# Kernel optimization log

Measured on AMD Instinct MI355X. Metric: run time of the kernel, lower is better.

Reference implementation:

```python
import jax, jax.numpy as jnp
import numpy as np

B, T, D, E, H, K = 4, 4096, 1024, 8, 512, 2  # batch, seq, n_embed, num_experts, bottleneck, top_k


def setup_inputs() -> dict:
    key = jax.random.key(0)
    ks = jax.random.split(key, 8)
    s = 0.02  # param scale (original zero-inits adapters; random used for a meaningful baseline)
    return {
        "x": jax.random.normal(ks[0], (B, T, D), jnp.float32),
        "Wr": (jax.random.normal(ks[1], (D, E), jnp.float32) * s),
        "br": jnp.zeros((E,), jnp.float32),
        "Wn": (jax.random.normal(ks[2], (D, E), jnp.float32) * s),
        "bn": jnp.zeros((E,), jnp.float32),
        "Wd": (jax.random.normal(ks[3], (E, D, H), jnp.float32) * s),
        "bd": jnp.zeros((E, H), jnp.float32),
        "Wu": (jax.random.normal(ks[4], (E, H, D), jnp.float32) * s),
        "bu": jnp.zeros((E, D), jnp.float32),
        "noise": jax.random.normal(ks[5], (B, T, E), jnp.float32),
        "top_k": K,
    }


def reference(x, Wr, br, Wn, bn, Wd, bd, Wu, bu, noise, top_k):
    # --- NoisyTopkRouter ---
    logits = x @ Wr + br                                   # [B,T,E]
    noise_logits = x @ Wn + bn                             # [B,T,E]
    noisy = logits + noise * jax.nn.softplus(noise_logits)  # randn * softplus(noise_logits)
    _, idx = jax.lax.top_k(noisy, top_k)                   # [B,T,K]
    # mask of selected experts; where(mask, noisy, -inf) == scatter(top_k_logits into -inf)
    mask = jax.nn.one_hot(idx, noisy.shape[-1], dtype=jnp.bool_).any(axis=-2)  # [B,T,E]
    sparse = jnp.where(mask, noisy, -jnp.inf)
    gates = jax.nn.softmax(sparse, axis=-1)                # zeros for unselected experts

    # --- Experts (dense grouped form; gate==0 exactly kills unselected experts incl. biases) ---
    down = jnp.einsum('btd,edh->bteh', x, Wd) + bd         # [B,T,E,H]
    hidden = jax.nn.gelu(down, approximate=False)          # torch GELU is exact (erf)
    up = jnp.einsum('bteh,ehd->bted', hidden, Wu) + bu     # [B,T,E,D]
    return jnp.einsum('bted,bte->btd', up, gates)          # gate-weighted combine
```

## Files before the change

### kernel.cpp

```cpp
#include <hip/hip_runtime.h>
#include <hip/hip_bf16.h>
#include <hip/hip_fp16.h>
#include <math.h>

#define DD   1024
#define EE   8
#define HH   512
#define NTOK 16384
#define MAXMT 40
#define NSL_D 4
#define NSL_U 8
#define NWD  (EE * MAXMT * NSL_D)
#define NWU  (EE * MAXMT * NSL_U)

typedef __attribute__((ext_vector_type(8))) short short8;
typedef __attribute__((ext_vector_type(4))) float floatx4;

__device__ __forceinline__ ushort f2bfu(float f) {
    __hip_bfloat16 h = __float2bfloat16(f);
    return *reinterpret_cast<ushort*>(&h);
}
__device__ __forceinline__ float bfu2f(ushort u) {
    union { unsigned u; float f; } cv; cv.u = ((unsigned)u) << 16; return cv.f;
}

__device__ __forceinline__ void glds16(const void* g, void* l) {
    __builtin_amdgcn_global_load_lds(
        (const __attribute__((address_space(1))) unsigned int*)g,
        (__attribute__((address_space(3))) unsigned int*)l, 16, 0, 0);
}

__global__ __launch_bounds__(256) void trans_k(const float* __restrict__ src, ushort* __restrict__ dst,
                                               const int R, const int C, int* __restrict__ cnt) {
    if (cnt && blockIdx.x == 0 && blockIdx.y == 0 && blockIdx.z == 0 && threadIdx.x < 256)
        cnt[threadIdx.x] = 0;
    const int e = blockIdx.z, r0 = blockIdx.y * 64, c0 = blockIdx.x * 64;
    __shared__ float t[64][65];
    const int tid = threadIdx.x;
    const int cseg = (tid & 15) * 4, rr = tid >> 4;
#pragma unroll
    for (int j = 0; j < 4; ++j) {
        const int r = rr + j * 16;
        const float4 v = *(const float4*)(src + ((size_t)e * R + r0 + r) * C + c0 + cseg);
        t[r][cseg] = v.x; t[r][cseg+1] = v.y; t[r][cseg+2] = v.z; t[r][cseg+3] = v.w;
    }
    __syncthreads();
    const int rseg = (tid & 15) * 4;
#pragma unroll
    for (int j = 0; j < 4; ++j) {
        const int crow = (tid >> 4) + j * 16;
        ushort o[4];
#pragma unroll
        for (int q = 0; q < 4; ++q) o[q] = f2bfu(t[rseg + q][crow]);
        *(uint2*)(dst + ((size_t)e * C + c0 + crow) * R + r0 + rseg) = *(uint2*)o;
    }
}

__device__ __forceinline__ void route_token(
    const float* ar, const float* an, int t,
    const float* __restrict__ br, const float* __restrict__ bn,
    const float* __restrict__ noise,
    unsigned& e0, unsigned& p0, unsigned& e1, unsigned& p1)
{
    float noisy[EE];
#pragma unroll
    for (int e = 0; e < EE; ++e) {
        const float lg = ar[e] + br[e];
        const float nl = an[e] + bn[e];
        const float sp = fmaxf(nl, 0.f) + log1pf(expf(-fabsf(nl)));
        noisy[e] = lg + noise[(size_t)t * EE + e] * sp;
    }
    int i0 = 0;
#pragma unroll
    for (int e = 1; e < EE; ++e) if (noisy[e] > noisy[i0]) i0 = e;
    int i1 = (i0 == 0) ? 1 : 0;
#pragma unroll
    for (int e = 0; e < EE; ++e) if (e != i0 && noisy[e] > noisy[i1]) i1 = e;
    const float ex = expf(noisy[i1] - noisy[i0]);
    const float g0 = 1.f / (1.f + ex);
    const float g1 = ex / (1.f + ex);
    __half h0 = __float2half_rn(g0), h1 = __float2half_rn(g1);
    e0 = (unsigned)i0;
    e1 = (unsigned)i1;
    p0 = (unsigned)t | ((unsigned)*reinterpret_cast<ushort*>(&h0) << 16);
    p1 = (unsigned)t | (1u << 14) | ((unsigned)*reinterpret_cast<ushort*>(&h1) << 16);
}

__global__ __launch_bounds__(512) void router_k(
    const float* __restrict__ x, const float* __restrict__ Wr, const float* __restrict__ br,
    const float* __restrict__ Wn, const float* __restrict__ bn, const float* __restrict__ noise,
    int* __restrict__ cnt, unsigned* __restrict__ entries, ushort* __restrict__ xb)
{
    __shared__ __align__(16) float WT[DD * 20];

    const int tid = threadIdx.x;
    {
        const int d0 = tid * 2;
#pragma unroll
        for (int r = 0; r < 2; ++r) {
            const int d = d0 + r;
            float4 a = *(const float4*)(Wr + (size_t)d * EE);
            float4 b = *(const float4*)(Wr + (size_t)d * EE + 4);
            float4 c = *(const float4*)(Wn + (size_t)d * EE);
            float4 e4 = *(const float4*)(Wn + (size_t)d * EE + 4);
            float* row = &WT[d * 20];
            *(float4*)(row + 0)  = a;
            *(float4*)(row + 4)  = b;
            *(float4*)(row + 8)  = c;
            *(float4*)(row + 12) = e4;
        }
    }
    __syncthreads();

    const int wave = tid >> 6;
    const int lane = tid & 63;
    const int t0 = blockIdx.x * 16 + wave * 2;

    float a0r[EE], a0n[EE], a1r[EE], a1n[EE];
#pragma unroll
    for (int e = 0; e < EE; ++e) { a0r[e] = 0.f; a0n[e] = 0.f; a1r[e] = 0.f; a1n[e] = 0.f; }

    const float* xr0 = x + (size_t)t0 * DD;
    const float* xr1 = xr0 + DD;
    ushort* xb0 = xb + (size_t)t0 * DD;
    ushort* xb1 = xb0 + DD;

#pragma unroll 4
    for (int s = 0; s < DD / 64; ++s) {
        const int d = s * 64 + lane;
        const float x0 = xr0[d];
        const float x1 = xr1[d];
        xb0[d] = f2bfu(x0);
        xb1[d] = f2bfu(x1);
        const float* row = &WT[d * 20];
        const float4 w0 = *(const float4*)(row + 0);
        const float4 w1 = *(const float4*)(row + 4);
        const float4 w2 = *(const float4*)(row + 8);
        const float4 w3 = *(const float4*)(row + 12);
        const float wr[8] = { w0.x, w0.y, w0.z, w0.w, w1.x, w1.y, w1.z, w1.w };
        const float wn[8] = { w2.x, w2.y, w2.z, w2.w, w3.x, w3.y, w3.z, w3.w };
#pragma unroll
        for (int e = 0; e < EE; ++e) {
            a0r[e] = fmaf(x0, wr[e], a0r[e]);
            a0n[e] = fmaf(x0, wn[e], a0n[e]);
            a1r[e] = fmaf(x1, wr[e], a1r[e]);
            a1n[e] = fmaf(x1, wn[e], a1n[e]);
        }
    }
#pragma unroll
    for (int off = 32; off > 0; off >>= 1) {
#pragma unroll
        for (int e = 0; e < EE; ++e) {
            a0r[e] += __shfl_xor(a0r[e], off);
            a0n[e] += __shfl_xor(a0n[e], off);
            a1r[e] += __shfl_xor(a1r[e], off);
            a1n[e] += __shfl_xor(a1n[e], off);
        }
    }

    unsigned e0a, p0a, e1a, p1a, e0b, p0b, e1b, p1b;
    if (lane == 0) {
        route_token(a0r, a0n, t0,     br, bn, noise, e0a, p0a, e1a, p1a);
        route_token(a1r, a1n, t0 + 1, br, bn, noise, e0b, p0b, e1b, p1b);
    }

    __syncthreads();
    unsigned* aggp = (unsigned*)WT;
    unsigned* agge = aggp + 32;
    if (lane == 0) {
        const int b = wave * 4;
        aggp[b + 0] = p0a; agge[b + 0] = e0a;
        aggp[b + 1] = p1a; agge[b + 1] = e1a;
        aggp[b + 2] = p0b; agge[b + 2] = e0b;
        aggp[b + 3] = p1b; agge[b + 3] = e1b;
    }
    __syncthreads();
    if (tid < EE) {
        int c = 0;
#pragma unroll
        for (int j = 0; j < 32; ++j) c += (agge[j] == (unsigned)tid);
        if (c) {
            int base = atomicAdd(&cnt[tid * 16], c);
            for (int j = 0; j < 32; ++j)
                if (agge[j] == (unsigned)tid) entries[tid * NTOK + (base++)] = aggp[j];
        }
    }
}


__global__ __launch_bounds__(256) void down_k(
    const ushort* __restrict__ xb, const ushort* __restrict__ WdT, const float* __restrict__ bd,
    const int* __restrict__ cnt, const unsigned* __restrict__ entries, ushort* __restrict__ hid)
{
    const int bx = blockIdx.x;
    const int wid = (bx & 7) * (NWD >> 3) + (bx >> 3);
    const int n0 = (wid % NSL_D) * 128;
    const int tile = wid / NSL_D;
    const int tm = tile % MAXMT;
    const int g = tile / MAXMT, e = g;
    const int n_g = cnt[g * 16];
    if (tm * 128 >= n_g) return;

    int og = 0;
    for (int gg = 0; gg < g; ++gg) og += cnt[gg * 16];

    __shared__ __align__(16) ushort As[2 * 128 * 64];
    __shared__ __align__(16) ushort Bs[2 * 128 * 64];
    __shared__ unsigned ecache[128];

    const int tid = threadIdx.x, lane = tid & 63, w = tid >> 6;
    const int wm = w >> 1, wn = w & 1;
    const int fr = lane & 15, fq = lane >> 4;

    if (tid < 128) {
        const int ridx = min(tm * 128 + tid, n_g - 1);
        ecache[tid] = entries[g * NTOK + ridx];
    }
    __syncthreads();

    const int lr = lane >> 3, seg = lane & 7;
    const int slog = seg ^ lr;
    const ushort* gA[4]; const ushort* gB[4];
    int loff[4];
    const ushort* WTe = WdT + (size_t)e * HH * DD;
#pragma unroll
    for (int j = 0; j < 4; ++j) {
        const int row = w * 32 + j * 8 + lr;
        const int tok = (int)(ecache[row] & 0x3FFFu);
        gA[j] = xb + (size_t)tok * DD + slog * 8;
        gB[j] = WTe + (size_t)(n0 + row) * DD + slog * 8;
        loff[j] = (w * 256 + j * 64) * 16;
    }

    floatx4 acc[4][4];
#pragma unroll
    for (int i = 0; i < 4; ++i)
#pragma unroll
        for (int j = 0; j < 4; ++j) acc[i][j] = (floatx4){0.f, 0.f, 0.f, 0.f};

    const int axr = wm * 64 + fr;
    const int bxr = wn * 64 + fr;

#pragma unroll
    for (int j = 0; j < 4; ++j) {
        glds16(gA[j], (char*)As + loff[j]);
        glds16(gB[j], (char*)Bs + loff[j]);
    }

    int cur = 0;
    for (int k0 = 0; k0 < DD; k0 += 64) {
        if (k0 + 64 < DD) {
            const int nb = (cur ^ 1) * 16384;
#pragma unroll
            for (int j = 0; j < 4; ++j) {
                glds16(gA[j] + k0 + 64, (char*)As + nb + loff[j]);
                glds16(gB[j] + k0 + 64, (char*)Bs + nb + loff[j]);
            }
            asm volatile("s_waitcnt vmcnt(8)" ::: "memory");
        } else {
            asm volatile("s_waitcnt vmcnt(0)" ::: "memory");
        }
        __builtin_amdgcn_sched_barrier(0);
        __builtin_amdgcn_s_barrier();
        asm volatile("" ::: "memory");
        const int cb = cur * 8192;
        __builtin_amdgcn_s_setprio(1);
#pragma unroll
        for (int kh = 0; kh < 2; ++kh) {
            short8 a[4], b[4];
#pragma unroll
            for (int mt = 0; mt < 4; ++mt) {
                const int r = axr + mt * 16;
                a[mt] = *(const short8*)&As[cb + r * 64 + ((kh * 4 + fq) ^ (r & 7)) * 8];
            }
#pragma unroll
            for (int nt = 0; nt < 4; ++nt) {
                const int r = bxr + nt * 16;
                b[nt] = *(const short8*)&Bs[cb + r * 64 + ((kh * 4 + fq) ^ (r & 7)) * 8];
            }
#pragma unroll
            for (int mt = 0; mt < 4; ++mt)
#pragma unroll
                for (int nt = 0; nt < 4; ++nt)
                    acc[mt][nt] = __builtin_amdgcn_mfma_f32_16x16x32_bf16(a[mt], b[nt], acc[mt][nt], 0, 0, 0);
        }
        __builtin_amdgcn_s_setprio(0);
        asm volatile("" ::: "memory");
        __builtin_amdgcn_s_barrier();
        cur ^= 1;
    }

    const int hbase = og + tm * 128;
#pragma unroll
    for (int nt = 0; nt < 4; ++nt) {
        const int n = n0 + wn * 64 + nt * 16 + fr;
        const float bias = bd[e * HH + n];
#pragma unroll
        for (int mt = 0; mt < 4; ++mt)
#pragma unroll
            for (int i = 0; i < 4; ++i) {
                const int rl = wm * 64 + mt * 16 + fq * 4 + i;
                if (tm * 128 + rl < n_g) {
                    const float v = acc[mt][nt][i] + bias;
                    const float ge = 0.5f * v * (1.f + erff(v * 0.7071067811865475f));
                    hid[(size_t)(hbase + rl) * HH + n] = f2bfu(ge);
                }
            }
    }
}

__global__ __launch_bounds__(256) void up_k(
    const ushort* __restrict__ hid, const ushort* __restrict__ WuT, const float* __restrict__ bu,
    const int* __restrict__ cnt, const unsigned* __restrict__ entries, ushort* __restrict__ slots)
{
    const int bx = blockIdx.x;
    const int wid = (bx & 7) * (NWU >> 3) + (bx >> 3);
    const int n0 = (wid % NSL_U) * 128;
    const int tile = wid / NSL_U;
    const int tm = tile % MAXMT;
    const int g = tile / MAXMT, e = g;
    const int n_g = cnt[g * 16];
    if (tm * 128 >= n_g) return;

    int hbase = 0;
    for (int gg = 0; gg < g; ++gg) hbase += cnt[gg * 16];

    __shared__ __align__(16) ushort As[2 * 128 * 64];
    __shared__ __align__(16) ushort Bs[2 * 128 * 64];
    __shared__ unsigned ecache[128];

    const int tid = threadIdx.x, lane = tid & 63, w = tid >> 6;
    const int wm = w >> 1, wn = w & 1;
    const int fr = lane & 15, fq = lane >> 4;

    if (tid < 128) {
        const int ridx = min(tm * 128 + tid, n_g - 1);
        ecache[tid] = entries[g * NTOK + ridx];
    }
    __syncthreads();

    const int lr = lane >> 3, seg = lane & 7;
    const int slog = seg ^ lr;
    const ushort* gA[4]; const ushort* gB[4];
    int loff[4];
    const ushort* WTe = WuT + (size_t)e * DD * HH;
#pragma unroll
    for (int j = 0; j < 4; ++j) {
        const int row = w * 32 + j * 8 + lr;
        const int ar = min(tm * 128 + row, n_g - 1);
        gA[j] = hid + (size_t)(hbase + ar) * HH + slog * 8;
        gB[j] = WTe + (size_t)(n0 + row) * HH + slog * 8;
        loff[j] = (w * 256 + j * 64) * 16;
    }

    floatx4 acc[4][4];
#pragma unroll
    for (int i = 0; i < 4; ++i)
#pragma unroll
        for (int j = 0; j < 4; ++j) acc[i][j] = (floatx4){0.f, 0.f, 0.f, 0.f};

    const int axr = wm * 64 + fr;
    const int bxr = wn * 64 + fr;

#pragma unroll
    for (int j = 0; j < 4; ++j) {
        glds16(gA[j], (char*)As + loff[j]);
        glds16(gB[j], (char*)Bs + loff[j]);
    }

    int cur = 0;
    for (int k0 = 0; k0 < HH; k0 += 64) {
        if (k0 + 64 < HH) {
            const int nb = (cur ^ 1) * 16384;
#pragma unroll
            for (int j = 0; j < 4; ++j) {
                glds16(gA[j] + k0 + 64, (char*)As + nb + loff[j]);
                glds16(gB[j] + k0 + 64, (char*)Bs + nb + loff[j]);
            }
            asm volatile("s_waitcnt vmcnt(8)" ::: "memory");
        } else {
            asm volatile("s_waitcnt vmcnt(0)" ::: "memory");
        }
        __builtin_amdgcn_sched_barrier(0);
        __builtin_amdgcn_s_barrier();
        asm volatile("" ::: "memory");
        const int cb = cur * 8192;
        __builtin_amdgcn_s_setprio(1);
#pragma unroll
        for (int kh = 0; kh < 2; ++kh) {
            short8 a[4], b[4];
#pragma unroll
            for (int mt = 0; mt < 4; ++mt) {
                const int r = axr + mt * 16;
                a[mt] = *(const short8*)&As[cb + r * 64 + ((kh * 4 + fq) ^ (r & 7)) * 8];
            }
#pragma unroll
            for (int nt = 0; nt < 4; ++nt) {
                const int r = bxr + nt * 16;
                b[nt] = *(const short8*)&Bs[cb + r * 64 + ((kh * 4 + fq) ^ (r & 7)) * 8];
            }
#pragma unroll
            for (int mt = 0; mt < 4; ++mt)
#pragma unroll
                for (int nt = 0; nt < 4; ++nt)
                    acc[mt][nt] = __builtin_amdgcn_mfma_f32_16x16x32_bf16(a[mt], b[nt], acc[mt][nt], 0, 0, 0);
        }
        __builtin_amdgcn_s_setprio(0);
        asm volatile("" ::: "memory");
        __builtin_amdgcn_s_barrier();
        cur ^= 1;
    }

#pragma unroll
    for (int nt = 0; nt < 4; ++nt) {
        const int n = n0 + wn * 64 + nt * 16 + fr;
        const float bias = bu[e * DD + n];
#pragma unroll
        for (int mt = 0; mt < 4; ++mt)
#pragma unroll
            for (int i = 0; i < 4; ++i) {
                const int rl = wm * 64 + mt * 16 + fq * 4 + i;
                if (tm * 128 + rl < n_g) {
                    const unsigned en = ecache[rl];
                    const int tok = (int)(en & 0x3FFFu);
                    const int slot = (int)((en >> 14) & 1u);
                    ushort hb = (ushort)(en >> 16);
                    const float gate = __half2float(*reinterpret_cast<__half*>(&hb));
                    const float v = (acc[mt][nt][i] + bias) * gate;
                    slots[((size_t)tok * 2 + slot) * DD + n] = f2bfu(v);
                }
            }
    }
}

__global__ __launch_bounds__(256) void combine_k(
    const ushort* __restrict__ slots, float* __restrict__ out)
{
    const size_t flat = ((size_t)blockIdx.x * 256 + threadIdx.x) * 8;
    const size_t t = flat >> 10;
    const size_t d = flat & (DD - 1);
    union { uint4 v; ushort h[8]; } a, b;
    a.v = *(const uint4*)(slots + ((t * 2 + 0) << 10) + d);
    b.v = *(const uint4*)(slots + ((t * 2 + 1) << 10) + d);
    float o[8];
#pragma unroll
    for (int j = 0; j < 8; ++j) o[j] = bfu2f(a.h[j]) + bfu2f(b.h[j]);
    *(float4*)(out + flat) = *(const float4*)&o[0];
    *(float4*)(out + flat + 4) = *(const float4*)&o[4];
}

extern "C" void kernel_launch(void* const* d_in, const int* in_sizes, int n_in,
                              void* d_out, int out_size, void* d_ws, size_t ws_size,
                              hipStream_t stream)
{
    const float* x     = (const float*)d_in[0];
    const float* Wr    = (const float*)d_in[1];
    const float* br    = (const float*)d_in[2];
    const float* Wn    = (const float*)d_in[3];
    const float* bn    = (const float*)d_in[4];
    const float* Wd    = (const float*)d_in[5];
    const float* bd    = (const float*)d_in[6];
    const float* Wu    = (const float*)d_in[7];
    const float* bu    = (const float*)d_in[8];
    const float* noise = (const float*)d_in[9];

    char* ws = (char*)d_ws;
    int*      cnt     = (int*)(ws + 0);
    unsigned* entries = (unsigned*)(ws + 2048);
    ushort*   xb      = (ushort*)(ws + 1050624);
    ushort*   WdT     = (ushort*)(ws + 34605056);
    ushort*   WuT     = (ushort*)(ws + 42993664);
    ushort*   hid     = (ushort*)(ws + 51382272);
    ushort*   slots   = (ushort*)(ws + 84936704);

    trans_k<<<dim3(HH / 64, DD / 64, EE), 256, 0, stream>>>(Wd, WdT, DD, HH, cnt);
    trans_k<<<dim3(DD / 64, HH / 64, EE), 256, 0, stream>>>(Wu, WuT, HH, DD, nullptr);
    router_k<<<NTOK / 16, 512, 0, stream>>>(x, Wr, br, Wn, bn, noise, cnt, entries, xb);
    down_k<<<NWD, 256, 0, stream>>>(xb, WdT, bd, cnt, entries, hid);
    up_k<<<NWU, 256, 0, stream>>>(hid, WuT, bu, cnt, entries, slots);
    combine_k<<<(NTOK * DD) / (256 * 8), 256, 0, stream>>>(slots, (float*)d_out);
}
```

Measured before the change: 431.8 us.

## Enlarge grouped GEMM tiles to 256x256 with 8-wave blocks

The down and up expert GEMMs move from 128x128 tiles with 4 waves to 256x256 tiles with 8 waves (512 threads). Each wave now computes a 128x64 sub-tile, which doubles reuse of each LDS fragment and cuts the number of blocks and global loads per FLOP. In exchange the LDS footprint doubles to 128 KB per block, more accumulator registers are needed, and padding waste grows for the last tile of each expert. The s_setprio hints are also removed.

```diff
diff --git a/kernel.cpp b/kernel.cpp
--- a/kernel.cpp
+++ b/kernel.cpp
@@ -7,11 +7,9 @@
 #define EE   8
 #define HH   512
 #define NTOK 16384
-#define MAXMT 40
-#define NSL_D 4
-#define NSL_U 8
-#define NWD  (EE * MAXMT * NSL_D)
-#define NWU  (EE * MAXMT * NSL_U)
+#define MT   20
+#define NWD  (EE * MT * 2)
+#define NWU  (EE * MT * 4)
 
 typedef __attribute__((ext_vector_type(8))) short short8;
 typedef __attribute__((ext_vector_type(4))) float floatx4;
@@ -188,32 +186,32 @@
 }
 
 
-__global__ __launch_bounds__(256) void down_k(
+__global__ __launch_bounds__(512, 2) void down_k(
     const ushort* __restrict__ xb, const ushort* __restrict__ WdT, const float* __restrict__ bd,
     const int* __restrict__ cnt, const unsigned* __restrict__ entries, ushort* __restrict__ hid)
 {
     const int bx = blockIdx.x;
     const int wid = (bx & 7) * (NWD >> 3) + (bx >> 3);
-    const int n0 = (wid % NSL_D) * 128;
-    const int tile = wid / NSL_D;
-    const int tm = tile % MAXMT;
-    const int g = tile / MAXMT, e = g;
+    const int n0 = (wid & 1) * 256;
+    const int tile = wid >> 1;
+    const int tm = tile % MT;
+    const int g = tile / MT, e = g;
     const int n_g = cnt[g * 16];
-    if (tm * 128 >= n_g) return;
+    if (tm * 256 >= n_g) return;
 
     int og = 0;
     for (int gg = 0; gg < g; ++gg) og += cnt[gg * 16];
 
-    __shared__ __align__(16) ushort As[2 * 128 * 64];
-    __shared__ __align__(16) ushort Bs[2 * 128 * 64];
-    __shared__ unsigned ecache[128];
+    __shared__ __align__(16) ushort As[2 * 256 * 64];
+    __shared__ __align__(16) ushort Bs[2 * 256 * 64];
+    __shared__ unsigned ecache[256];
 
     const int tid = threadIdx.x, lane = tid & 63, w = tid >> 6;
-    const int wm = w >> 1, wn = w & 1;
+    const int wm = w >> 2, wn = w & 3;
     const int fr = lane & 15, fq = lane >> 4;
 
-    if (tid < 128) {
-        const int ridx = min(tm * 128 + tid, n_g - 1);
+    if (tid < 256) {
+        const int ridx = min(tm * 256 + tid, n_g - 1);
         ecache[tid] = entries[g * NTOK + ridx];
     }
     __syncthreads();
@@ -229,16 +227,16 @@
         const int tok = (int)(ecache[row] & 0x3FFFu);
         gA[j] = xb + (size_t)tok * DD + slog * 8;
         gB[j] = WTe + (size_t)(n0 + row) * DD + slog * 8;
-        loff[j] = (w * 256 + j * 64) * 16;
-    }
-
-    floatx4 acc[4][4];
-#pragma unroll
-    for (int i = 0; i < 4; ++i)
+        loff[j] = (w * 32 + j * 8) * 128;
+    }
+
+    floatx4 acc[8][4];
+#pragma unroll
+    for (int i = 0; i < 8; ++i)
 #pragma unroll
         for (int j = 0; j < 4; ++j) acc[i][j] = (floatx4){0.f, 0.f, 0.f, 0.f};
 
-    const int axr = wm * 64 + fr;
+    const int axr = wm * 128 + fr;
     const int bxr = wn * 64 + fr;
 
 #pragma unroll
@@ -250,7 +248,7 @@
     int cur = 0;
     for (int k0 = 0; k0 < DD; k0 += 64) {
         if (k0 + 64 < DD) {
-            const int nb = (cur ^ 1) * 16384;
+            const int nb = (cur ^ 1) * 32768;
 #pragma unroll
             for (int j = 0; j < 4; ++j) {
                 glds16(gA[j] + k0 + 64, (char*)As + nb + loff[j]);
@@ -263,13 +261,12 @@
         __builtin_amdgcn_sched_barrier(0);
         __builtin_amdgcn_s_barrier();
         asm volatile("" ::: "memory");
-        const int cb = cur * 8192;
-        __builtin_amdgcn_s_setprio(1);
+        const int cb = cur * 16384;
 #pragma unroll
         for (int kh = 0; kh < 2; ++kh) {
-            short8 a[4], b[4];
-#pragma unroll
-            for (int mt = 0; mt < 4; ++mt) {
+            short8 a[8], b[4];
+#pragma unroll
+            for (int mt = 0; mt < 8; ++mt) {
                 const int r = axr + mt * 16;
                 a[mt] = *(const short8*)&As[cb + r * 64 + ((kh * 4 + fq) ^ (r & 7)) * 8];
             }
@@ -279,28 +276,27 @@
                 b[nt] = *(const short8*)&Bs[cb + r * 64 + ((kh * 4 + fq) ^ (r & 7)) * 8];
             }
 #pragma unroll
-            for (int mt = 0; mt < 4; ++mt)
+            for (int mt = 0; mt < 8; ++mt)
 #pragma unroll
                 for (int nt = 0; nt < 4; ++nt)
                     acc[mt][nt] = __builtin_amdgcn_mfma_f32_16x16x32_bf16(a[mt], b[nt], acc[mt][nt], 0, 0, 0);
         }
-        __builtin_amdgcn_s_setprio(0);
         asm volatile("" ::: "memory");
         __builtin_amdgcn_s_barrier();
         cur ^= 1;
     }
 
-    const int hbase = og + tm * 128;
+    const int hbase = og + tm * 256;
 #pragma unroll
     for (int nt = 0; nt < 4; ++nt) {
         const int n = n0 + wn * 64 + nt * 16 + fr;
         const float bias = bd[e * HH + n];
 #pragma unroll
-        for (int mt = 0; mt < 4; ++mt)
+        for (int mt = 0; mt < 8; ++mt)
 #pragma unroll
             for (int i = 0; i < 4; ++i) {
-                const int rl = wm * 64 + mt * 16 + fq * 4 + i;
-                if (tm * 128 + rl < n_g) {
+                const int rl = wm * 128 + mt * 16 + fq * 4 + i;
+                if (tm * 256 + rl < n_g) {
                     const float v = acc[mt][nt][i] + bias;
                     const float ge = 0.5f * v * (1.f + erff(v * 0.7071067811865475f));
                     hid[(size_t)(hbase + rl) * HH + n] = f2bfu(ge);
@@ -309,32 +305,32 @@
     }
 }
 
-__global__ __launch_bounds__(256) void up_k(
+__global__ __launch_bounds__(512, 2) void up_k(
     const ushort* __restrict__ hid, const ushort* __restrict__ WuT, const float* __restrict__ bu,
     const int* __restrict__ cnt, const unsigned* __restrict__ entries, ushort* __restrict__ slots)
 {
     const int bx = blockIdx.x;
     const int wid = (bx & 7) * (NWU >> 3) + (bx >> 3);
-    const int n0 = (wid % NSL_U) * 128;
-    const int tile = wid / NSL_U;
-    const int tm = tile % MAXMT;
-    const int g = tile / MAXMT, e = g;
+    const int n0 = (wid & 3) * 256;
+    const int tile = wid >> 2;
+    const int tm = tile % MT;
+    const int g = tile / MT, e = g;
     const int n_g = cnt[g * 16];
-    if (tm * 128 >= n_g) return;
+    if (tm * 256 >= n_g) return;
 
     int hbase = 0;
     for (int gg = 0; gg < g; ++gg) hbase += cnt[gg * 16];
 
-    __shared__ __align__(16) ushort As[2 * 128 * 64];
-    __shared__ __align__(16) ushort Bs[2 * 128 * 64];
-    __shared__ unsigned ecache[128];
+    __shared__ __align__(16) ushort As[2 * 256 * 64];
+    __shared__ __align__(16) ushort Bs[2 * 256 * 64];
+    __shared__ unsigned ecache[256];
 
     const int tid = threadIdx.x, lane = tid & 63, w = tid >> 6;
-    const int wm = w >> 1, wn = w & 1;
+    const int wm = w >> 2, wn = w & 3;
     const int fr = lane & 15, fq = lane >> 4;
 
-    if (tid < 128) {
-        const int ridx = min(tm * 128 + tid, n_g - 1);
+    if (tid < 256) {
+        const int ridx = min(tm * 256 + tid, n_g - 1);
         ecache[tid] = entries[g * NTOK + ridx];
     }
     __syncthreads();
@@ -347,19 +343,19 @@
 #pragma unroll
     for (int j = 0; j < 4; ++j) {
         const int row = w * 32 + j * 8 + lr;
-        const int ar = min(tm * 128 + row, n_g - 1);
+        const int ar = min(tm * 256 + row, n_g - 1);
         gA[j] = hid + (size_t)(hbase + ar) * HH + slog * 8;
         gB[j] = WTe + (size_t)(n0 + row) * HH + slog * 8;
-        loff[j] = (w * 256 + j * 64) * 16;
-    }
-
-    floatx4 acc[4][4];
-#pragma unroll
-    for (int i = 0; i < 4; ++i)
+        loff[j] = (w * 32 + j * 8) * 128;
+    }
+
+    floatx4 acc[8][4];
+#pragma unroll
+    for (int i = 0; i < 8; ++i)
 #pragma unroll
         for (int j = 0; j < 4; ++j) acc[i][j] = (floatx4){0.f, 0.f, 0.f, 0.f};
 
-    const int axr = wm * 64 + fr;
+    const int axr = wm * 128 + fr;
     const int bxr = wn * 64 + fr;
 
 #pragma unroll
@@ -371,7 +367,7 @@
     int cur = 0;
     for (int k0 = 0; k0 < HH; k0 += 64) {
         if (k0 + 64 < HH) {
-            const int nb = (cur ^ 1) * 16384;
+            const int nb = (cur ^ 1) * 32768;
 #pragma unroll
             for (int j = 0; j < 4; ++j) {
                 glds16(gA[j] + k0 + 64, (char*)As + nb + loff[j]);
@@ -384,13 +380,12 @@
         __builtin_amdgcn_sched_barrier(0);
         __builtin_amdgcn_s_barrier();
         asm volatile("" ::: "memory");
-        const int cb = cur * 8192;
-        __builtin_amdgcn_s_setprio(1);
+        const int cb = cur * 16384;
 #pragma unroll
         for (int kh = 0; kh < 2; ++kh) {
-            short8 a[4], b[4];
-#pragma unroll
-            for (int mt = 0; mt < 4; ++mt) {
+            short8 a[8], b[4];
+#pragma unroll
+            for (int mt = 0; mt < 8; ++mt) {
                 const int r = axr + mt * 16;
                 a[mt] = *(const short8*)&As[cb + r * 64 + ((kh * 4 + fq) ^ (r & 7)) * 8];
             }
@@ -400,12 +395,11 @@
                 b[nt] = *(const short8*)&Bs[cb + r * 64 + ((kh * 4 + fq) ^ (r & 7)) * 8];
             }
 #pragma unroll
-            for (int mt = 0; mt < 4; ++mt)
+            for (int mt = 0; mt < 8; ++mt)
 #pragma unroll
                 for (int nt = 0; nt < 4; ++nt)
                     acc[mt][nt] = __builtin_amdgcn_mfma_f32_16x16x32_bf16(a[mt], b[nt], acc[mt][nt], 0, 0, 0);
         }
-        __builtin_amdgcn_s_setprio(0);
         asm volatile("" ::: "memory");
         __builtin_amdgcn_s_barrier();
         cur ^= 1;
@@ -416,11 +410,11 @@
         const int n = n0 + wn * 64 + nt * 16 + fr;
         const float bias = bu[e * DD + n];
 #pragma unroll
-        for (int mt = 0; mt < 4; ++mt)
+        for (int mt = 0; mt < 8; ++mt)
 #pragma unroll
             for (int i = 0; i < 4; ++i) {
-                const int rl = wm * 64 + mt * 16 + fq * 4 + i;
-                if (tm * 128 + rl < n_g) {
+                const int rl = wm * 128 + mt * 16 + fq * 4 + i;
+                if (tm * 256 + rl < n_g) {
                     const unsigned en = ecache[rl];
                     const int tok = (int)(en & 0x3FFFu);
                     const int slot = (int)((en >> 14) & 1u);
@@ -476,7 +470,7 @@
     trans_k<<<dim3(HH / 64, DD / 64, EE), 256, 0, stream>>>(Wd, WdT, DD, HH, cnt);
     trans_k<<<dim3(DD / 64, HH / 64, EE), 256, 0, stream>>>(Wu, WuT, HH, DD, nullptr);
     router_k<<<NTOK / 16, 512, 0, stream>>>(x, Wr, br, Wn, bn, noise, cnt, entries, xb);
-    down_k<<<NWD, 256, 0, stream>>>(xb, WdT, bd, cnt, entries, hid);
-    up_k<<<NWU, 256, 0, stream>>>(hid, WuT, bu, cnt, entries, slots);
+    down_k<<<NWD, 512, 0, stream>>>(xb, WdT, bd, cnt, entries, hid);
+    up_k<<<NWU, 512, 0, stream>>>(hid, WuT, bu, cnt, entries, slots);
     combine_k<<<(NTOK * DD) / (256 * 8), 256, 0, stream>>>(slots, (float*)d_out);
 }
```

Measured after the change: 463.4 us. 7.3% more time.

## Fuse top-k combine into up-projection via float atomics and merge transpose kernels

Applied to the files above, without the earlier changes.

The up-projection now atomically adds gate-weighted fp32 results straight into the zeroed output instead of writing bf16 per-slot buffers, which removes the separate combine kernel and the slots buffer round trip. The two weight-transpose launches are merged into one kernel over a 16x16x16 grid, where some blocks exit early, and a memset zeroes the output first. In exchange it adds roughly 33M scattered float atomics and a 64MB memset. Summation order between the two experts becomes nondeterministic.

```diff
diff --git a/kernel.cpp b/kernel.cpp
--- a/kernel.cpp
+++ b/kernel.cpp
@@ -30,11 +30,19 @@
         (__attribute__((address_space(3))) unsigned int*)l, 16, 0, 0);
 }
 
-__global__ __launch_bounds__(256) void trans_k(const float* __restrict__ src, ushort* __restrict__ dst,
-                                               const int R, const int C, int* __restrict__ cnt) {
-    if (cnt && blockIdx.x == 0 && blockIdx.y == 0 && blockIdx.z == 0 && threadIdx.x < 256)
+__global__ __launch_bounds__(256) void trans2_k(
+    const float* __restrict__ Wd, ushort* __restrict__ WdT,
+    const float* __restrict__ Wu, ushort* __restrict__ WuT,
+    int* __restrict__ cnt)
+{
+    if (blockIdx.x == 0 && blockIdx.y == 0 && blockIdx.z == 0 && threadIdx.x < 256)
         cnt[threadIdx.x] = 0;
-    const int e = blockIdx.z, r0 = blockIdx.y * 64, c0 = blockIdx.x * 64;
+    const int z = blockIdx.z;
+    const float* src; ushort* dst; int R, C, e;
+    if (z < EE) { src = Wd; dst = WdT; R = DD; C = HH; e = z; }
+    else        { src = Wu; dst = WuT; R = HH; C = DD; e = z - EE; }
+    if ((int)blockIdx.x >= C / 64 || (int)blockIdx.y >= R / 64) return;
+    const int r0 = blockIdx.y * 64, c0 = blockIdx.x * 64;
     __shared__ float t[64][65];
     const int tid = threadIdx.x;
     const int cseg = (tid & 15) * 4, rr = tid >> 4;
@@ -311,7 +319,7 @@
 
 __global__ __launch_bounds__(256) void up_k(
     const ushort* __restrict__ hid, const ushort* __restrict__ WuT, const float* __restrict__ bu,
-    const int* __restrict__ cnt, const unsigned* __restrict__ entries, ushort* __restrict__ slots)
+    const int* __restrict__ cnt, const unsigned* __restrict__ entries, float* __restrict__ out)
 {
     const int bx = blockIdx.x;
     const int wid = (bx & 7) * (NWU >> 3) + (bx >> 3);
@@ -423,30 +431,12 @@
                 if (tm * 128 + rl < n_g) {
                     const unsigned en = ecache[rl];
                     const int tok = (int)(en & 0x3FFFu);
-                    const int slot = (int)((en >> 14) & 1u);
                     ushort hb = (ushort)(en >> 16);
                     const float gate = __half2float(*reinterpret_cast<__half*>(&hb));
-                    const float v = (acc[mt][nt][i] + bias) * gate;
-                    slots[((size_t)tok * 2 + slot) * DD + n] = f2bfu(v);
+                    atomicAdd(out + (size_t)tok * DD + n, (acc[mt][nt][i] + bias) * gate);
                 }
             }
     }
-}
-
-__global__ __launch_bounds__(256) void combine_k(
-    const ushort* __restrict__ slots, float* __restrict__ out)
-{
-    const size_t flat = ((size_t)blockIdx.x * 256 + threadIdx.x) * 8;
-    const size_t t = flat >> 10;
-    const size_t d = flat & (DD - 1);
-    union { uint4 v; ushort h[8]; } a, b;
-    a.v = *(const uint4*)(slots + ((t * 2 + 0) << 10) + d);
-    b.v = *(const uint4*)(slots + ((t * 2 + 1) << 10) + d);
-    float o[8];
-#pragma unroll
-    for (int j = 0; j < 8; ++j) o[j] = bfu2f(a.h[j]) + bfu2f(b.h[j]);
-    *(float4*)(out + flat) = *(const float4*)&o[0];
-    *(float4*)(out + flat + 4) = *(const float4*)&o[4];
 }
 
 extern "C" void kernel_launch(void* const* d_in, const int* in_sizes, int n_in,
@@ -471,12 +461,10 @@
     ushort*   WdT     = (ushort*)(ws + 34605056);
     ushort*   WuT     = (ushort*)(ws + 42993664);
     ushort*   hid     = (ushort*)(ws + 51382272);
-    ushort*   slots   = (ushort*)(ws + 84936704);
-
-    trans_k<<<dim3(HH / 64, DD / 64, EE), 256, 0, stream>>>(Wd, WdT, DD, HH, cnt);
-    trans_k<<<dim3(DD / 64, HH / 64, EE), 256, 0, stream>>>(Wu, WuT, HH, DD, nullptr);
+
+    hipMemsetAsync(d_out, 0, out_size, stream);
+    trans2_k<<<dim3(16, 16, 16), 256, 0, stream>>>(Wd, WdT, Wu, WuT, cnt);
     router_k<<<NTOK / 16, 512, 0, stream>>>(x, Wr, br, Wn, bn, noise, cnt, entries, xb);
     down_k<<<NWD, 256, 0, stream>>>(xb, WdT, bd, cnt, entries, hid);
-    up_k<<<NWU, 256, 0, stream>>>(hid, WuT, bu, cnt, entries, slots);
-    combine_k<<<(NTOK * DD) / (256 * 8), 256, 0, stream>>>(slots, (float*)d_out);
-}
+    up_k<<<NWU, 256, 0, stream>>>(hid, WuT, bu, cnt, entries, (float*)d_out);
+}
```

Measured after the change: 537.5 us. 1.24x slower.
